# Kernel tuning notes

Measured on AMD Instinct MI355X. Metric: run time of the kernel, lower is better.

Reference implementation:

```python
import jax, jax.numpy as jnp
import numpy as np

N_HEADS = 16

def setup_inputs() -> dict:
    key = jax.random.key(0)
    ks = jax.random.split(key, 5)
    d_model = 1024
    init_scale = 0.02
    x = jax.random.normal(ks[0], (2, 2048, d_model), dtype=jnp.float32)
    wq = init_scale * jax.random.normal(ks[1], (d_model, d_model), dtype=jnp.float32)
    wk = init_scale * jax.random.normal(ks[2], (d_model, d_model), dtype=jnp.float32)
    wv = init_scale * jax.random.normal(ks[3], (d_model, d_model), dtype=jnp.float32)
    wo = init_scale * jax.random.normal(ks[4], (d_model, d_model), dtype=jnp.float32)
    return {"x": x, "wq": wq, "wk": wk, "wv": wv, "wo": wo}

def reference(x, wq, wk, wv, wo):
    # x: [B, S, D]; weights: [D, D] applied as x @ W.T (torch nn.Parameter convention)
    B, S, D = x.shape
    H = N_HEADS
    hd = D // H
    q = (x @ wq.T).reshape(B, S, H, hd).transpose(0, 2, 1, 3)  # [B,H,S,hd]
    k = (x @ wk.T).reshape(B, S, H, hd).transpose(0, 2, 1, 3)
    v = (x @ wv.T).reshape(B, S, H, hd).transpose(0, 2, 1, 3)
    scores = jnp.einsum('bhqd,bhkd->bhqk', q, k) / jnp.sqrt(jnp.float32(hd))
    # causal mask: mask out k > q (past_length = 0)
    causal = jnp.triu(jnp.ones((S, S), dtype=bool), k=1)
    scores = jnp.where(causal[None, None], -jnp.inf, scores)
    attn = jax.nn.softmax(scores, axis=-1)
    # dropout is identity in eval mode (training=False)
    out = jnp.einsum('bhqk,bhkd->bhqd', attn, v)  # [B,H,S,hd]
    out = out.transpose(0, 2, 1, 3).reshape(B, S, D)
    return out @ wo.T
```

## Files before the change

kernel.cpp:

```cpp
#include <hip/hip_runtime.h>
#include <hip/hip_bf16.h>


#define DEVI __device__ __forceinline__

typedef __attribute__((ext_vector_type(4))) float f32x4;
typedef __attribute__((ext_vector_type(8))) short s16x8;

static constexpr int SEQ = 2048;
static constexpr int DM  = 1024;
static constexpr int NH  = 16;
static constexpr int HD  = 64;
static constexpr int LDQKV = 3072;

DEVI short f2bf(float f) {
  __hip_bfloat16 h = __float2bfloat16(f);
  return *(short*)&h;
}

__global__ void cast_kernel(const float* __restrict__ in, short* __restrict__ out, int n4) {
  int i = blockIdx.x * blockDim.x + threadIdx.x;
  if (i >= n4) return;
  float4 v = ((const float4*)in)[i];
  short4 o;
  o.x = f2bf(v.x); o.y = f2bf(v.y); o.z = f2bf(v.z); o.w = f2bf(v.w);
  ((short4*)out)[i] = o;
}

__global__ void cast4_kernel(const float* __restrict__ w0, const float* __restrict__ w1,
                             const float* __restrict__ w2, const float* __restrict__ w3,
                             short* __restrict__ o012, short* __restrict__ o3) {
  int seg = blockIdx.x >> 10;
  int i = (blockIdx.x & 1023) * blockDim.x + threadIdx.x;
  const float* src = (seg == 0) ? w0 : (seg == 1) ? w1 : (seg == 2) ? w2 : w3;
  short* dst = (seg == 3) ? o3 : (o012 + (size_t)seg * (1u << 20));
  float4 v = ((const float4*)src)[i];
  short4 o;
  o.x = f2bf(v.x); o.y = f2bf(v.y); o.z = f2bf(v.z); o.w = f2bf(v.w);
  ((short4*)dst)[i] = o;
}

template<bool BF16_OUT>
__global__ __launch_bounds__(256) void gemm_nt(const short* __restrict__ A,
                                               const short* __restrict__ Bm,
                                               void* __restrict__ Cv,
                                               int M, int N, int K,
                                               int qcols, float qscale) {
  __shared__ short As[128 * 32];
  __shared__ short Bs[128 * 32];
  const int t = threadIdx.x;
  const int l = t & 63;
  const int w = t >> 6;
  const int wr = w >> 1, wc = w & 1;
  const int lr = l & 15, lg = l >> 4;
  const int m0 = blockIdx.y * 128, n0 = blockIdx.x * 128;
  f32x4 acc[4][4] = {};

  for (int k0 = 0; k0 < K; k0 += 32) {
    __syncthreads();
#pragma unroll
    for (int i = 0; i < 2; ++i) {
      int idx = t * 8 + i * 2048;
      int row = idx >> 5, col = idx & 31;
      __builtin_amdgcn_global_load_lds(
          (const __attribute__((address_space(1))) void*)(A + (size_t)(m0 + row) * K + k0 + col),
          (__attribute__((address_space(3))) void*)(As + idx), 16, 0, 0);
      __builtin_amdgcn_global_load_lds(
          (const __attribute__((address_space(1))) void*)(Bm + (size_t)(n0 + row) * K + k0 + col),
          (__attribute__((address_space(3))) void*)(Bs + idx), 16, 0, 0);
    }
    __syncthreads();

    s16x8 af[4], bfr[4];
#pragma unroll
    for (int i = 0; i < 4; ++i)
      af[i] = *(const s16x8*)&As[(wr * 64 + i * 16 + lr) * 32 + lg * 8];
#pragma unroll
    for (int j = 0; j < 4; ++j)
      bfr[j] = *(const s16x8*)&Bs[(wc * 64 + j * 16 + lr) * 32 + lg * 8];
#pragma unroll
    for (int i = 0; i < 4; ++i)
#pragma unroll
      for (int j = 0; j < 4; ++j)
        acc[i][j] = __builtin_amdgcn_mfma_f32_16x16x32_bf16(af[i], bfr[j], acc[i][j], 0, 0, 0);
  }

  const float s = (n0 < qcols) ? qscale : 1.0f;
#pragma unroll
  for (int i = 0; i < 4; ++i)
#pragma unroll
    for (int j = 0; j < 4; ++j)
#pragma unroll
      for (int r = 0; r < 4; ++r) {
        int row = m0 + wr * 64 + i * 16 + lg * 4 + r;
        int col = n0 + wc * 64 + j * 16 + lr;
        if constexpr (BF16_OUT)
          ((short*)Cv)[(size_t)row * N + col] = f2bf(acc[i][j][r] * s);
        else
          ((float*)Cv)[(size_t)row * N + col] = acc[i][j][r] * s;
      }
}

__global__ __launch_bounds__(256) void attn_kernel(const unsigned short* __restrict__ QKV,
                                                   unsigned short* __restrict__ O) {
  __shared__ short Ks[64 * 72];
  __shared__ short Vt[64 * 72];
  __shared__ short Ps[64 * 72];

  const int t = threadIdx.x, l = t & 63, w = t >> 6;
  const int lr = l & 15, lg = l >> 4;
  const int bid = blockIdx.x;
  const int bh = bid & 31;
  const int g  = (bid >> 5) & 7;
  const int rr = bid >> 8;
  const int qt = (rr == 0) ? g : (rr == 1) ? 31 - g : (rr == 2) ? 8 + g : 23 - g;
  const int b = bh >> 4, h = bh & 15;
  const int q0 = qt * 64;
  const size_t rowbase = (size_t)b * SEQ * LDQKV;
  const int cb = h * HD;
  const unsigned short* Q = QKV + cb;
  const unsigned short* K = QKV + DM + cb;
  const unsigned short* V = QKV + 2 * DM + cb;

  s16x8 qf[2];
  {
    const unsigned short* qp = Q + rowbase + (size_t)(q0 + w * 16 + lr) * LDQKV + lg * 8;
    qf[0] = *(const s16x8*)(qp);
    qf[1] = *(const s16x8*)(qp + 32);
  }

  f32x4 acc[4] = {};
  float mrun[4], lrun[4];
#pragma unroll
  for (int r = 0; r < 4; ++r) { mrun[r] = -3.0e38f; lrun[r] = 0.f; }

  s16x8 kA, kB, vA, vB;
  {
    const unsigned short* kp = K + rowbase + (size_t)l * LDQKV + w * 16;
    kA = *(const s16x8*)kp;
    kB = *(const s16x8*)(kp + 8);
    const unsigned short* vp = V + rowbase + (size_t)l * LDQKV + w * 16;
    vA = *(const s16x8*)vp;
    vB = *(const s16x8*)(vp + 8);
  }

  for (int kt = 0; kt <= qt; ++kt) {
    const int kv0 = kt * 64;
    __syncthreads();

    *(s16x8*)&Ks[l * 72 + w * 16] = kA;
    *(s16x8*)&Ks[l * 72 + w * 16 + 8] = kB;
#pragma unroll
    for (int jj = 0; jj < 8; ++jj) Vt[(w * 16 + jj) * 72 + l] = vA[jj];
#pragma unroll
    for (int jj = 0; jj < 8; ++jj) Vt[(w * 16 + 8 + jj) * 72 + l] = vB[jj];

    {
      const int nkv = (kt < qt) ? kv0 + 64 : kv0;
      const unsigned short* kp = K + rowbase + (size_t)(nkv + l) * LDQKV + w * 16;
      kA = *(const s16x8*)kp;
      kB = *(const s16x8*)(kp + 8);
      const unsigned short* vp = V + rowbase + (size_t)(nkv + l) * LDQKV + w * 16;
      vA = *(const s16x8*)vp;
      vB = *(const s16x8*)(vp + 8);
    }

    asm volatile("s_waitcnt lgkmcnt(0)" ::: "memory");
    __builtin_amdgcn_s_barrier();

    f32x4 sc[4] = {};
    __builtin_amdgcn_s_setprio(1);
#pragma unroll
    for (int dk = 0; dk < 2; ++dk)
#pragma unroll
      for (int j = 0; j < 4; ++j) {
        s16x8 kb = *(const s16x8*)&Ks[(j * 16 + lr) * 72 + dk * 32 + lg * 8];
        sc[j] = __builtin_amdgcn_mfma_f32_16x16x32_bf16(qf[dk], kb, sc[j], 0, 0, 0);
      }
    __builtin_amdgcn_s_setprio(0);

    if (kt == qt) {
#pragma unroll
      for (int j = 0; j < 4; ++j)
#pragma unroll
        for (int r = 0; r < 4; ++r) {
          int kg = kv0 + j * 16 + lr;
          int qg = q0 + w * 16 + lg * 4 + r;
          if (kg > qg) sc[j][r] = -3.0e38f;
        }
    }

    float lmax[4];
#pragma unroll
    for (int r = 0; r < 4; ++r)
      lmax[r] = fmaxf(fmaxf(sc[0][r], sc[1][r]), fmaxf(sc[2][r], sc[3][r]));
    bool need = false;
#pragma unroll
    for (int r = 0; r < 4; ++r) need |= (lmax[r] > mrun[r] + 8.0f);
    if (__any(need)) {
#pragma unroll
      for (int r = 0; r < 4; ++r) {
        float m = lmax[r];
#pragma unroll
        for (int mk = 1; mk < 16; mk <<= 1) m = fmaxf(m, __shfl_xor(m, mk, 64));
        float mnew = fmaxf(mrun[r], m);
        float corr = exp2f(mrun[r] - mnew);
        mrun[r] = mnew;
        lrun[r] *= corr;
#pragma unroll
        for (int j = 0; j < 4; ++j) acc[j][r] *= corr;
      }
    }

#pragma unroll
    for (int r = 0; r < 4; ++r) {
      float rsum = 0.f;
#pragma unroll
      for (int j = 0; j < 4; ++j) {
        float p = exp2f(sc[j][r] - mrun[r]);
        sc[j][r] = p;
        rsum += p;
      }
      lrun[r] += rsum;
    }

#pragma unroll
    for (int j = 0; j < 4; ++j)
#pragma unroll
      for (int r = 0; r < 4; ++r)
        Ps[(w * 16 + lg * 4 + r) * 72 + j * 16 + lr] = f2bf(sc[j][r]);

    __builtin_amdgcn_s_setprio(1);
#pragma unroll
    for (int ks = 0; ks < 2; ++ks) {
      s16x8 pa = *(const s16x8*)&Ps[(w * 16 + lr) * 72 + ks * 32 + lg * 8];
#pragma unroll
      for (int j = 0; j < 4; ++j) {
        s16x8 vb = *(const s16x8*)&Vt[(j * 16 + lr) * 72 + ks * 32 + lg * 8];
        acc[j] = __builtin_amdgcn_mfma_f32_16x16x32_bf16(pa, vb, acc[j], 0, 0, 0);
      }
    }
    __builtin_amdgcn_s_setprio(0);
  }

#pragma unroll
  for (int r = 0; r < 4; ++r) {
    float ls = lrun[r];
#pragma unroll
    for (int mk = 1; mk < 16; mk <<= 1) ls += __shfl_xor(ls, mk, 64);
    lrun[r] = ls;
  }
#pragma unroll
  for (int j = 0; j < 4; ++j)
#pragma unroll
    for (int r = 0; r < 4; ++r) {
      int qg = q0 + w * 16 + lg * 4 + r;
      float o = acc[j][r] / lrun[r];
      O[(size_t)b * SEQ * DM + (size_t)qg * DM + cb + j * 16 + lr] = (unsigned short)f2bf(o);
    }
}

extern "C" void kernel_launch(void* const* d_in, const int* in_sizes, int n_in,
                              void* d_out, int out_size, void* d_ws, size_t ws_size,
                              hipStream_t stream) {
  const float* x  = (const float*)d_in[0];
  const float* wq = (const float*)d_in[1];
  const float* wk = (const float*)d_in[2];
  const float* wv = (const float*)d_in[3];
  const float* wo = (const float*)d_in[4];
  float* out = (float*)d_out;

  short* ws   = (short*)d_ws;
  short* xb   = ws;
  short* wqkv = xb   + (4u << 20);
  short* wob  = wqkv + (3u << 20);
  short* QKV  = wob  + (1u << 20);
  short* Om   = QKV  + (12u << 20);

  cast_kernel<<<4096, 256, 0, stream>>>(x, xb, 1 << 20);
  cast4_kernel<<<4096, 256, 0, stream>>>(wq, wk, wv, wo, wqkv, wob);

  const float SCL = 0.125f * 1.4426950408889634f;
  gemm_nt<true><<<dim3(24, 32), 256, 0, stream>>>(xb, wqkv, QKV, 4096, LDQKV, 1024,
                                                  DM, SCL);

  attn_kernel<<<1024, 256, 0, stream>>>((const unsigned short*)QKV,
                                        (unsigned short*)Om);

  gemm_nt<false><<<dim3(8, 32), 256, 0, stream>>>(Om, wob, out, 4096, 1024, 1024,
                                                  0, 1.0f);
}
```

Before: 201.0 us.

## Deepen GEMM K-tile, add 64-row GEMM variant, use 128-query attention tiles

The GEMM K step grows from 32 to 64, which halves the number of barrier rounds. A BM template parameter lets the output projection use 64-row tiles, so it launches twice as many blocks. The attention kernel now uses 512-thread blocks that each cover 128 query rows with eight waves, so each staged K/V tile is shared by more query rows and the work is split into 512 blocks. In exchange, shared memory and register pressure go up, the causal mask is applied per wave, and the attention grid has fewer blocks to balance across CUs.

```diff
diff --git a/kernel.cpp b/kernel.cpp
--- a/kernel.cpp
+++ b/kernel.cpp
@@ -40,60 +40,72 @@
   ((short4*)dst)[i] = o;
 }
 
-template<bool BF16_OUT>
+template<int BM, bool BF16_OUT>
 __global__ __launch_bounds__(256) void gemm_nt(const short* __restrict__ A,
                                                const short* __restrict__ Bm,
                                                void* __restrict__ Cv,
                                                int M, int N, int K,
                                                int qcols, float qscale) {
-  __shared__ short As[128 * 32];
-  __shared__ short Bs[128 * 32];
+  __shared__ short As[BM * 64];
+  __shared__ short Bs[128 * 64];
+  constexpr int WCN = (BM == 128) ? 2 : 4;
+  constexpr int WTN = 128 / WCN;
+  constexpr int FC  = WTN / 16;
   const int t = threadIdx.x;
   const int l = t & 63;
   const int w = t >> 6;
-  const int wr = w >> 1, wc = w & 1;
+  const int wr = (BM == 128) ? (w >> 1) : 0;
+  const int wc = (BM == 128) ? (w & 1) : w;
   const int lr = l & 15, lg = l >> 4;
-  const int m0 = blockIdx.y * 128, n0 = blockIdx.x * 128;
-  f32x4 acc[4][4] = {};
-
-  for (int k0 = 0; k0 < K; k0 += 32) {
+  const int m0 = blockIdx.y * BM, n0 = blockIdx.x * 128;
+  f32x4 acc[4][FC] = {};
+
+  for (int k0 = 0; k0 < K; k0 += 64) {
     __syncthreads();
 #pragma unroll
-    for (int i = 0; i < 2; ++i) {
+    for (int i = 0; i < BM / 32; ++i) {
       int idx = t * 8 + i * 2048;
-      int row = idx >> 5, col = idx & 31;
+      int row = idx >> 6, col = idx & 63;
       __builtin_amdgcn_global_load_lds(
           (const __attribute__((address_space(1))) void*)(A + (size_t)(m0 + row) * K + k0 + col),
           (__attribute__((address_space(3))) void*)(As + idx), 16, 0, 0);
+    }
+#pragma unroll
+    for (int i = 0; i < 4; ++i) {
+      int idx = t * 8 + i * 2048;
+      int row = idx >> 6, col = idx & 63;
       __builtin_amdgcn_global_load_lds(
           (const __attribute__((address_space(1))) void*)(Bm + (size_t)(n0 + row) * K + k0 + col),
           (__attribute__((address_space(3))) void*)(Bs + idx), 16, 0, 0);
     }
     __syncthreads();
 
-    s16x8 af[4], bfr[4];
-#pragma unroll
-    for (int i = 0; i < 4; ++i)
-      af[i] = *(const s16x8*)&As[(wr * 64 + i * 16 + lr) * 32 + lg * 8];
-#pragma unroll
-    for (int j = 0; j < 4; ++j)
-      bfr[j] = *(const s16x8*)&Bs[(wc * 64 + j * 16 + lr) * 32 + lg * 8];
-#pragma unroll
-    for (int i = 0; i < 4; ++i)
-#pragma unroll
-      for (int j = 0; j < 4; ++j)
-        acc[i][j] = __builtin_amdgcn_mfma_f32_16x16x32_bf16(af[i], bfr[j], acc[i][j], 0, 0, 0);
+#pragma unroll
+    for (int kk = 0; kk < 2; ++kk) {
+      s16x8 af[4], bfr[FC];
+#pragma unroll
+      for (int i = 0; i < 4; ++i)
+        af[i] = *(const s16x8*)&As[(wr * 64 + i * 16 + lr) * 64 + kk * 32 + lg * 8];
+#pragma unroll
+      for (int j = 0; j < FC; ++j)
+        bfr[j] = *(const s16x8*)&Bs[(wc * WTN + j * 16 + lr) * 64 + kk * 32 + lg * 8];
+#pragma unroll
+      for (int i = 0; i < 4; ++i)
+#pragma unroll
+        for (int j = 0; j < FC; ++j)
+          acc[i][j] = __builtin_amdgcn_mfma_f32_16x16x32_bf16(af[i], bfr[j], acc[i][j], 0, 0, 0);
+    }
   }
 
   const float s = (n0 < qcols) ? qscale : 1.0f;
 #pragma unroll
   for (int i = 0; i < 4; ++i)
 #pragma unroll
-    for (int j = 0; j < 4; ++j)
+    for (int j = 0; j < FC; ++j)
 #pragma unroll
       for (int r = 0; r < 4; ++r) {
         int row = m0 + wr * 64 + i * 16 + lg * 4 + r;
-        int col = n0 + wc * 64 + j * 16 + lr;
+        int col = n0 + wc * WTN + j * 16 + lr;
         if constexpr (BF16_OUT)
           ((short*)Cv)[(size_t)row * N + col] = f2bf(acc[i][j][r] * s);
         else
@@ -101,21 +113,22 @@
       }
 }
 
-__global__ __launch_bounds__(256) void attn_kernel(const unsigned short* __restrict__ QKV,
+__global__ __launch_bounds__(512) void attn_kernel(const unsigned short* __restrict__ QKV,
                                                    unsigned short* __restrict__ O) {
   __shared__ short Ks[64 * 72];
   __shared__ short Vt[64 * 72];
-  __shared__ short Ps[64 * 72];
+  __shared__ short Ps[128 * 72];
 
   const int t = threadIdx.x, l = t & 63, w = t >> 6;
   const int lr = l & 15, lg = l >> 4;
   const int bid = blockIdx.x;
   const int bh = bid & 31;
   const int g  = (bid >> 5) & 7;
-  const int rr = bid >> 8;
-  const int qt = (rr == 0) ? g : (rr == 1) ? 31 - g : (rr == 2) ? 8 + g : 23 - g;
+  const int rr = (bid >> 8) & 1;
+  const int qt = rr ? 15 - g : g;
   const int b = bh >> 4, h = bh & 15;
-  const int q0 = qt * 64;
+  const int q0 = qt * 128;
+  const int ktmax = 2 * qt + 1;
   const size_t rowbase = (size_t)b * SEQ * LDQKV;
   const int cb = h * HD;
   const unsigned short* Q = QKV + cb;
@@ -134,35 +147,28 @@
 #pragma unroll
   for (int r = 0; r < 4; ++r) { mrun[r] = -3.0e38f; lrun[r] = 0.f; }
 
-  s16x8 kA, kB, vA, vB;
+  s16x8 kA, vA;
   {
-    const unsigned short* kp = K + rowbase + (size_t)l * LDQKV + w * 16;
+    const unsigned short* kp = K + rowbase + (size_t)l * LDQKV + w * 8;
     kA = *(const s16x8*)kp;
-    kB = *(const s16x8*)(kp + 8);
-    const unsigned short* vp = V + rowbase + (size_t)l * LDQKV + w * 16;
+    const unsigned short* vp = V + rowbase + (size_t)l * LDQKV + w * 8;
     vA = *(const s16x8*)vp;
-    vB = *(const s16x8*)(vp + 8);
-  }
-
-  for (int kt = 0; kt <= qt; ++kt) {
+  }
+
+  for (int kt = 0; kt <= ktmax; ++kt) {
     const int kv0 = kt * 64;
     __syncthreads();
 
-    *(s16x8*)&Ks[l * 72 + w * 16] = kA;
-    *(s16x8*)&Ks[l * 72 + w * 16 + 8] = kB;
-#pragma unroll
-    for (int jj = 0; jj < 8; ++jj) Vt[(w * 16 + jj) * 72 + l] = vA[jj];
-#pragma unroll
-    for (int jj = 0; jj < 8; ++jj) Vt[(w * 16 + 8 + jj) * 72 + l] = vB[jj];
+    *(s16x8*)&Ks[l * 72 + w * 8] = kA;
+#pragma unroll
+    for (int jj = 0; jj < 8; ++jj) Vt[(w * 8 + jj) * 72 + l] = vA[jj];
 
     {
-      const int nkv = (kt < qt) ? kv0 + 64 : kv0;
-      const unsigned short* kp = K + rowbase + (size_t)(nkv + l) * LDQKV + w * 16;
+      const int nkv = (kt < ktmax) ? kv0 + 64 : kv0;
+      const unsigned short* kp = K + rowbase + (size_t)(nkv + l) * LDQKV + w * 8;
       kA = *(const s16x8*)kp;
-      kB = *(const s16x8*)(kp + 8);
-      const unsigned short* vp = V + rowbase + (size_t)(nkv + l) * LDQKV + w * 16;
+      const unsigned short* vp = V + rowbase + (size_t)(nkv + l) * LDQKV + w * 8;
       vA = *(const s16x8*)vp;
-      vB = *(const s16x8*)(vp + 8);
     }
 
     asm volatile("s_waitcnt lgkmcnt(0)" ::: "memory");
@@ -179,7 +185,7 @@
       }
     __builtin_amdgcn_s_setprio(0);
 
-    if (kt == qt) {
+    if (kv0 + 63 > q0 + w * 16) {
 #pragma unroll
       for (int j = 0; j < 4; ++j)
 #pragma unroll
@@ -281,12 +287,12 @@
   cast4_kernel<<<4096, 256, 0, stream>>>(wq, wk, wv, wo, wqkv, wob);
 
   const float SCL = 0.125f * 1.4426950408889634f;
-  gemm_nt<true><<<dim3(24, 32), 256, 0, stream>>>(xb, wqkv, QKV, 4096, LDQKV, 1024,
-                                                  DM, SCL);
-
-  attn_kernel<<<1024, 256, 0, stream>>>((const unsigned short*)QKV,
-                                        (unsigned short*)Om);
-
-  gemm_nt<false><<<dim3(8, 32), 256, 0, stream>>>(Om, wob, out, 4096, 1024, 1024,
-                                                  0, 1.0f);
-}
+  gemm_nt<128, true><<<dim3(24, 32), 256, 0, stream>>>(xb, wqkv, QKV, 4096, LDQKV, 1024,
+                                                       DM, SCL);
+
+  attn_kernel<<<512, 512, 0, stream>>>((const unsigned short*)QKV,
+                                       (unsigned short*)Om);
+
+  gemm_nt<64, false><<<dim3(8, 64), 256, 0, stream>>>(Om, wob, out, 4096, 1024, 1024,
+                                                      0, 1.0f);
+}
```

Result: slower. 210.8 us (+4.9%).

## Use 128-row query tiles, load K fragments directly into registers, double-buffer V

Applied to the files above, without the earlier changes.

The attention kernel now runs 8 waves per block over a 128-row query tile and launches half as many blocks. K MFMA operands are loaded straight from global memory into registers, which drops the K shared-memory staging. V uses a two-slot shared buffer, so each tile needs only one barrier. The key loop is unrolled by two. The cost is more registers and redundant global K reads per wave, and each row range now processes up to 64 fully masked keys at the diagonal.

```diff
diff --git a/kernel.cpp b/kernel.cpp
--- a/kernel.cpp
+++ b/kernel.cpp
@@ -101,85 +101,72 @@
       }
 }
 
-__global__ __launch_bounds__(256) void attn_kernel(const unsigned short* __restrict__ QKV,
-                                                   unsigned short* __restrict__ O) {
-  __shared__ short Ks[64 * 72];
-  __shared__ short Vt[64 * 72];
-  __shared__ short Ps[64 * 72];
+__global__ __launch_bounds__(512, 4) void attn_kernel(const unsigned short* __restrict__ QKV,
+                                                      unsigned short* __restrict__ O) {
+  __shared__ short Vt[2][64 * 72];
+  __shared__ short Ps[128 * 72];
 
   const int t = threadIdx.x, l = t & 63, w = t >> 6;
   const int lr = l & 15, lg = l >> 4;
   const int bid = blockIdx.x;
   const int bh = bid & 31;
   const int g  = (bid >> 5) & 7;
-  const int rr = bid >> 8;
-  const int qt = (rr == 0) ? g : (rr == 1) ? 31 - g : (rr == 2) ? 8 + g : 23 - g;
+  const int rr = (bid >> 8) & 1;
+  const int qt = rr ? 15 - g : g;
   const int b = bh >> 4, h = bh & 15;
-  const int q0 = qt * 64;
+  const int q0 = qt * 128;
+  const int ktmax = 2 * qt + 1;
   const size_t rowbase = (size_t)b * SEQ * LDQKV;
   const int cb = h * HD;
-  const unsigned short* Q = QKV + cb;
-  const unsigned short* K = QKV + DM + cb;
-  const unsigned short* V = QKV + 2 * DM + cb;
 
   s16x8 qf[2];
   {
-    const unsigned short* qp = Q + rowbase + (size_t)(q0 + w * 16 + lr) * LDQKV + lg * 8;
+    const unsigned short* qp = QKV + rowbase + cb + (size_t)(q0 + w * 16 + lr) * LDQKV + lg * 8;
     qf[0] = *(const s16x8*)(qp);
     qf[1] = *(const s16x8*)(qp + 32);
   }
 
+  const unsigned short* Kl = QKV + rowbase + DM + cb + (size_t)lr * LDQKV + lg * 8;
+  const unsigned short* Vl = QKV + rowbase + 2 * DM + cb + (size_t)l * LDQKV + w * 8;
+
   f32x4 acc[4] = {};
   float mrun[4], lrun[4];
 #pragma unroll
   for (int r = 0; r < 4; ++r) { mrun[r] = -3.0e38f; lrun[r] = 0.f; }
 
-  s16x8 kA, kB, vA, vB;
-  {
-    const unsigned short* kp = K + rowbase + (size_t)l * LDQKV + w * 16;
-    kA = *(const s16x8*)kp;
-    kB = *(const s16x8*)(kp + 8);
-    const unsigned short* vp = V + rowbase + (size_t)l * LDQKV + w * 16;
-    vA = *(const s16x8*)vp;
-    vB = *(const s16x8*)(vp + 8);
-  }
-
-  for (int kt = 0; kt <= qt; ++kt) {
+  s16x8 kf[2][4], vA, vB;
+  vA = *(const s16x8*)(Vl);
+#pragma unroll
+  for (int dk = 0; dk < 2; ++dk)
+#pragma unroll
+    for (int j = 0; j < 4; ++j)
+      kf[dk][j] = *(const s16x8*)(Kl + (size_t)(j * 16) * LDQKV + dk * 32);
+
+  auto tile = [&](int kt, s16x8& vcur, s16x8& vnxt, int p) {
     const int kv0 = kt * 64;
-    __syncthreads();
-
-    *(s16x8*)&Ks[l * 72 + w * 16] = kA;
-    *(s16x8*)&Ks[l * 72 + w * 16 + 8] = kB;
-#pragma unroll
-    for (int jj = 0; jj < 8; ++jj) Vt[(w * 16 + jj) * 72 + l] = vA[jj];
-#pragma unroll
-    for (int jj = 0; jj < 8; ++jj) Vt[(w * 16 + 8 + jj) * 72 + l] = vB[jj];
-
-    {
-      const int nkv = (kt < qt) ? kv0 + 64 : kv0;
-      const unsigned short* kp = K + rowbase + (size_t)(nkv + l) * LDQKV + w * 16;
-      kA = *(const s16x8*)kp;
-      kB = *(const s16x8*)(kp + 8);
-      const unsigned short* vp = V + rowbase + (size_t)(nkv + l) * LDQKV + w * 16;
-      vA = *(const s16x8*)vp;
-      vB = *(const s16x8*)(vp + 8);
-    }
-
-    asm volatile("s_waitcnt lgkmcnt(0)" ::: "memory");
-    __builtin_amdgcn_s_barrier();
+    const int nkv = (kt < ktmax) ? kv0 + 64 : kv0;
+
+#pragma unroll
+    for (int jj = 0; jj < 8; ++jj) Vt[p][(w * 8 + jj) * 72 + l] = vcur[jj];
+
+    vnxt = *(const s16x8*)(Vl + (size_t)nkv * LDQKV);
 
     f32x4 sc[4] = {};
     __builtin_amdgcn_s_setprio(1);
 #pragma unroll
     for (int dk = 0; dk < 2; ++dk)
 #pragma unroll
-      for (int j = 0; j < 4; ++j) {
-        s16x8 kb = *(const s16x8*)&Ks[(j * 16 + lr) * 72 + dk * 32 + lg * 8];
-        sc[j] = __builtin_amdgcn_mfma_f32_16x16x32_bf16(qf[dk], kb, sc[j], 0, 0, 0);
-      }
+      for (int j = 0; j < 4; ++j)
+        sc[j] = __builtin_amdgcn_mfma_f32_16x16x32_bf16(qf[dk], kf[dk][j], sc[j], 0, 0, 0);
     __builtin_amdgcn_s_setprio(0);
 
-    if (kt == qt) {
+#pragma unroll
+    for (int dk = 0; dk < 2; ++dk)
+#pragma unroll
+      for (int j = 0; j < 4; ++j)
+        kf[dk][j] = *(const s16x8*)(Kl + (size_t)(nkv + j * 16) * LDQKV + dk * 32);
+
+    if (kv0 + 63 > q0 + w * 16) {
 #pragma unroll
       for (int j = 0; j < 4; ++j)
 #pragma unroll
@@ -230,17 +217,25 @@
       for (int r = 0; r < 4; ++r)
         Ps[(w * 16 + lg * 4 + r) * 72 + j * 16 + lr] = f2bf(sc[j][r]);
 
+    asm volatile("s_waitcnt lgkmcnt(0)" ::: "memory");
+    __builtin_amdgcn_s_barrier();
+
     __builtin_amdgcn_s_setprio(1);
 #pragma unroll
     for (int ks = 0; ks < 2; ++ks) {
       s16x8 pa = *(const s16x8*)&Ps[(w * 16 + lr) * 72 + ks * 32 + lg * 8];
 #pragma unroll
       for (int j = 0; j < 4; ++j) {
-        s16x8 vb = *(const s16x8*)&Vt[(j * 16 + lr) * 72 + ks * 32 + lg * 8];
+        s16x8 vb = *(const s16x8*)&Vt[p][(j * 16 + lr) * 72 + ks * 32 + lg * 8];
         acc[j] = __builtin_amdgcn_mfma_f32_16x16x32_bf16(pa, vb, acc[j], 0, 0, 0);
       }
     }
     __builtin_amdgcn_s_setprio(0);
+  };
+
+  for (int kt = 0; kt <= ktmax; kt += 2) {
+    tile(kt,     vA, vB, 0);
+    tile(kt + 1, vB, vA, 1);
   }
 
 #pragma unroll
@@ -284,8 +279,8 @@
   gemm_nt<true><<<dim3(24, 32), 256, 0, stream>>>(xb, wqkv, QKV, 4096, LDQKV, 1024,
                                                   DM, SCL);
 
-  attn_kernel<<<1024, 256, 0, stream>>>((const unsigned short*)QKV,
-                                        (unsigned short*)Om);
+  attn_kernel<<<512, 512, 0, stream>>>((const unsigned short*)QKV,
+                                       (unsigned short*)Om);
 
   gemm_nt<false><<<dim3(8, 32), 256, 0, stream>>>(Om, wob, out, 4096, 1024, 1024,
                                                   0, 1.0f);
```

Result: slower. 222.2 us (+10.6%).
